# Kernel tuning notes

Measured on AMD Instinct MI355X. Metric: run time of the kernel, lower is better.

## Reference

```python
import jax, jax.numpy as jnp
import numpy as np

NEG_INF = -1e16


def setup_inputs() -> dict:
    key = jax.random.key(0)
    k1, k2, k3 = jax.random.split(key, 3)
    B, N, C, D = 8, 4096, 64, 64
    inputs = jax.random.normal(k1, (B, N, C), dtype=jnp.float32)
    graph = jax.random.randint(k2, (N, N), 0, 2, dtype=jnp.int32)
    # xavier_uniform for Linear weight [D, C]
    limit = float(np.sqrt(6.0 / (C + D)))
    W = jax.random.uniform(k3, (D, C), dtype=jnp.float32, minval=-limit, maxval=limit)
    b = jnp.zeros((D,), dtype=jnp.float32)
    return {"inputs": inputs, "graph": graph, "W": W, "b": b}


def reference(inputs, graph, W, b):
    # h = W(inputs): [B, N, D]
    h = jnp.einsum('bnc,dc->bnd', inputs, W)
    # dense pairwise scores: [B, N, N]
    scores = jnp.einsum('bnd,bmd->bnm', h, h)
    # mask non-edges (graph broadcasts over batch)
    scores = jnp.where(graph[None, :, :] == 0, NEG_INF, scores)
    attention = jax.nn.softmax(scores, axis=2)
    out = jnp.einsum('bnm,bmd->bnd', attention, h) + b
    return out
```

## Files before the change

kernel.cpp:

```cpp
#include <hip/hip_runtime.h>
#include <stdint.h>

typedef _Float16 f16x8 __attribute__((ext_vector_type(8)));
typedef _Float16 f16x4 __attribute__((ext_vector_type(4)));
typedef __fp16 half2_t __attribute__((ext_vector_type(2)));
typedef float f32x4 __attribute__((ext_vector_type(4)));

#define LOG2E 1.44269504088896340736f
#define NEGINF (-1e16f)

constexpr int kN = 4096;
constexpr int kD = 64;
constexpr int kB = 8;

__global__ __launch_bounds__(256) void hproj_kernel(const float* __restrict__ x,
                                                    const float* __restrict__ W,
                                                    _Float16* __restrict__ hout,
                                                    _Float16* __restrict__ hTout)
{
    __shared__ float Wt[64][64];
    __shared__ float xs[64][65];
    __shared__ _Float16 ht[64][68];

    const int tid = threadIdx.x;
    const int r   = tid >> 2;
    const int c0  = (tid & 3) * 16;

    #pragma unroll
    for (int j = 0; j < 16; j += 4) {
        const float4 v = *(const float4*)(W + r * 64 + c0 + j);
        Wt[c0 + j + 0][r] = v.x;
        Wt[c0 + j + 1][r] = v.y;
        Wt[c0 + j + 2][r] = v.z;
        Wt[c0 + j + 3][r] = v.w;
    }
    const long rowbase = (long)blockIdx.x * 64;
    #pragma unroll
    for (int j = 0; j < 16; j += 4) {
        const float4 v = *(const float4*)(x + (rowbase + r) * 64 + c0 + j);
        xs[r][c0 + j + 0] = v.x;
        xs[r][c0 + j + 1] = v.y;
        xs[r][c0 + j + 2] = v.z;
        xs[r][c0 + j + 3] = v.w;
    }
    __syncthreads();

    const int d0 = (tid & 3) * 16;
    f32x4 acc[4] = {{0.f,0.f,0.f,0.f},{0.f,0.f,0.f,0.f},{0.f,0.f,0.f,0.f},{0.f,0.f,0.f,0.f}};
    #pragma unroll 4
    for (int c = 0; c < 64; ++c) {
        const float xv = xs[r][c];
        const f32x4* wrow = (const f32x4*)&Wt[c][d0];
        #pragma unroll
        for (int k = 0; k < 4; ++k) acc[k] += wrow[k] * xv;
    }
    f16x8 o0, o1;
    #pragma unroll
    for (int j = 0; j < 8; ++j) {
        o0[j] = (_Float16)acc[j >> 2][j & 3];
        o1[j] = (_Float16)acc[2 + (j >> 2)][j & 3];
    }
    *(f16x8*)(hout + (rowbase + r) * 64 + d0)     = o0;
    *(f16x8*)(hout + (rowbase + r) * 64 + d0 + 8) = o1;

    #pragma unroll
    for (int j = 0; j < 8; ++j) {
        ht[r][d0 + j]     = o0[j];
        ht[r][d0 + 8 + j] = o1[j];
    }
    __syncthreads();

    const int bb = blockIdx.x >> 6;
    const int n0 = (int)(rowbase & (kN - 1));
    const int dr = tid >> 2;
    const int c4 = (tid & 3) * 16;
    f16x8 t0, t1;
    #pragma unroll
    for (int j = 0; j < 8; ++j) {
        t0[j] = ht[c4 + j][dr];
        t1[j] = ht[c4 + 8 + j][dr];
    }
    _Float16* dst = hTout + (long)bb * kD * kN + (long)dr * kN + n0 + c4;
    *(f16x8*)(dst)     = t0;
    *(f16x8*)(dst + 8) = t1;
}

__global__ __launch_bounds__(256) void graphmask_kernel(const int* __restrict__ g,
                                                        uint64_t* __restrict__ wmout)
{
    const int tid  = threadIdx.x;
    const int wv   = tid >> 6;
    const int lane = tid & 63;
    const int ll   = lane & 15;
    const int lg   = lane >> 4;
    const int pair = blockIdx.x * 4 + wv;
    const int q16  = pair >> 6;
    const int kv64 = pair & 63;

    const int* gr = g + (long)(q16 * 16 + ll) * kN + kv64 * 64 + 8 * lg;
    const int4 u0 = *(const int4*)(gr);
    const int4 u1 = *(const int4*)(gr + 4);
    const int4 u2 = *(const int4*)(gr + 32);
    const int4 u3 = *(const int4*)(gr + 36);

    int gv[16];
    gv[0] = u0.x;  gv[1] = u0.y;  gv[2] = u0.z;  gv[3] = u0.w;
    gv[4] = u1.x;  gv[5] = u1.y;  gv[6] = u1.z;  gv[7] = u1.w;
    gv[8] = u2.x;  gv[9] = u2.y;  gv[10] = u2.z;  gv[11] = u2.w;
    gv[12] = u3.x; gv[13] = u3.y; gv[14] = u3.z;  gv[15] = u3.w;

    uint64_t Wb[16];
    #pragma unroll
    for (int s = 0; s < 16; ++s) {
        const int t = s >> 2, rr = s & 3;
        const int j = (t >= 2 ? 8 : 0) + 4 * (t & 1) + rr;
        Wb[s] = __ballot(gv[j] != 0);
    }

    const int s = lane;
    uint64_t a0 = (s & 1) ? Wb[1]  : Wb[0];
    uint64_t a1 = (s & 1) ? Wb[3]  : Wb[2];
    uint64_t a2 = (s & 1) ? Wb[5]  : Wb[4];
    uint64_t a3 = (s & 1) ? Wb[7]  : Wb[6];
    uint64_t a4 = (s & 1) ? Wb[9]  : Wb[8];
    uint64_t a5 = (s & 1) ? Wb[11] : Wb[10];
    uint64_t a6 = (s & 1) ? Wb[13] : Wb[12];
    uint64_t a7 = (s & 1) ? Wb[15] : Wb[14];
    uint64_t b0 = (s & 2) ? a1 : a0;
    uint64_t b1 = (s & 2) ? a3 : a2;
    uint64_t b2 = (s & 2) ? a5 : a4;
    uint64_t b3 = (s & 2) ? a7 : a6;
    uint64_t c0 = (s & 4) ? b1 : b0;
    uint64_t c1 = (s & 4) ? b3 : b2;
    uint64_t v  = (s & 8) ? c1 : c0;
    if (lane < 16) wmout[(long)pair * 16 + lane] = v;
}

__global__ __launch_bounds__(512, 4) void attn_kernel(const _Float16* __restrict__ h,
                                                      const _Float16* __restrict__ hT,
                                                      const uint64_t* __restrict__ wmask,
                                                      const float* __restrict__ bias,
                                                      float* __restrict__ outp,
                                                      _Float16* __restrict__ pO,
                                                      float* __restrict__ pml,
                                                      int kvlen)
{
    __shared__ alignas(16) char Kl[2][8192];
    __shared__ alignas(16) char Vt[2][8192];

    const int b     = blockIdx.y;
    const int split = blockIdx.z;
    const int q0    = blockIdx.x * 256;
    const int tid   = threadIdx.x;
    const int wave  = tid >> 6;
    const int lane  = tid & 63;
    const int lg    = lane >> 4;
    const int ll    = lane & 15;

    const _Float16* hb  = h  + (long)b * kN * kD;
    const _Float16* hTb = hT + (long)b * kD * kN;
    const int kv_base = split * kvlen;
    const int NT      = kvlen / 64;

    const int qA = q0 + wave * 32 + ll;
    const int qB = qA + 16;
    const f16x8 qfA0 = *(const f16x8*)(hb + qA * 64 + lg * 8);
    const f16x8 qfA1 = *(const f16x8*)(hb + qA * 64 + 32 + lg * 8);
    const f16x8 qfB0 = *(const f16x8*)(hb + qB * 64 + lg * 8);
    const f16x8 qfB1 = *(const f16x8*)(hb + qB * 64 + 32 + lg * 8);

    f16x8 vone;
    {
        const _Float16 o = (ll == 0) ? (_Float16)1.0f : (_Float16)0.0f;
        #pragma unroll
        for (int j = 0; j < 8; ++j) vone[j] = o;
    }

    f32x4 OaccA[4] = {{0.f,0.f,0.f,0.f},{0.f,0.f,0.f,0.f},{0.f,0.f,0.f,0.f},{0.f,0.f,0.f,0.f}};
    f32x4 OaccB[4] = {{0.f,0.f,0.f,0.f},{0.f,0.f,0.f,0.f},{0.f,0.f,0.f,0.f},{0.f,0.f,0.f,0.f}};
    f32x4 Oacc4A = {0.f, 0.f, 0.f, 0.f};
    f32x4 Oacc4B = {0.f, 0.f, 0.f, 0.f};
    float m_runA = NEGINF, m_runB = NEGINF;
    float mmA = NEGINF * LOG2E, mmB = NEGINF * LOG2E;
    float negv = NEGINF;

    const int sr  = tid >> 3;
    const int sc8 = (tid & 7) * 8;
    const int srp = (sr & 0x23) | ((sr & 0x18) >> 1) | ((sr & 0x4) << 2);

    const int kw = srp * 128 + ((sc8 * 2) ^ ((srp & 7) << 4));
    const int vw = sr  * 128 + ((sc8 * 2) ^ ((sr  & 7) << 4));
    const int rb0 = ll * 128 + (((lg * 16))      ^ ((ll & 7) << 4));
    const int rb1 = ll * 128 + (((64 + lg * 16)) ^ ((ll & 7) << 4));

    char* const KB = (char*)Kl;
    char* const VB = (char*)Vt;

    const _Float16* gK = hb  + (long)(kv_base + sr) * 64 + sc8;
    const _Float16* gV = hTb + (long)sr * kN + kv_base + sc8;

    const int wuni = __builtin_amdgcn_readfirstlane(wave);
    const uint64_t* __restrict__ wmpA =
        wmask + ((long)(blockIdx.x * 16 + wuni * 2) * 64 + (kv_base >> 6)) * 16;
    const uint64_t* __restrict__ wmpB = wmpA + (long)64 * 16;

    {
        const f16x8 a0 = *(const f16x8*)(gK);
        const f16x8 b0 = *(const f16x8*)(gV);
        *(f16x8*)(KB + kw) = a0;
        *(f16x8*)(VB + vw) = b0;
        gK += 64 * 64;  gV += 64;
    }

    union PF { half2_t hh[4]; f16x8 v; };

#define SOFTMAX_FRAG(S_, WM_, OACC_, OACC4_, MRUN_, MM_, PF1_, PF2_)             \
    do {                                                                         \
        _Pragma("unroll")                                                        \
        for (int t = 0; t < 4; ++t) {                                            \
            _Pragma("unroll")                                                    \
            for (int rr = 0; rr < 4; ++rr) {                                     \
                float sv = S_[t][rr];                                            \
                asm("v_cndmask_b32 %0, %1, %2, %3"                               \
                    : "=v"(sv) : "v"(negv), "v"(sv), "s"(WM_[t * 4 + rr]));      \
                S_[t][rr] = sv;                                                  \
            }                                                                    \
        }                                                                        \
        float mx0 = fmaxf(fmaxf(S_[0][0], S_[0][1]), fmaxf(S_[0][2], S_[0][3])); \
        float mx1 = fmaxf(fmaxf(S_[1][0], S_[1][1]), fmaxf(S_[1][2], S_[1][3])); \
        float mx2 = fmaxf(fmaxf(S_[2][0], S_[2][1]), fmaxf(S_[2][2], S_[2][3])); \
        float mx3 = fmaxf(fmaxf(S_[3][0], S_[3][1]), fmaxf(S_[3][2], S_[3][3])); \
        float mloc = fmaxf(fmaxf(mx0, mx1), fmaxf(mx2, mx3));                    \
        mloc = fmaxf(mloc, __shfl_xor(mloc, 16));                                \
        mloc = fmaxf(mloc, __shfl_xor(mloc, 32));                                \
        if (__any(mloc > MRUN_ + 8.f)) {                                         \
            const float mnew = fmaxf(MRUN_, mloc);                               \
            const float scl  = __builtin_amdgcn_exp2f((MRUN_ - mnew) * LOG2E);   \
            MRUN_ = mnew;                                                        \
            MM_   = mnew * LOG2E;                                                \
            _Pragma("unroll")                                                    \
            for (int dt = 0; dt < 4; ++dt) OACC_[dt] *= scl;                     \
            OACC4_ *= scl;                                                       \
        }                                                                        \
        _Pragma("unroll")                                                        \
        for (int t = 0; t < 4; ++t) {                                            \
            _Pragma("unroll")                                                    \
            for (int rr = 0; rr < 4; ++rr)                                       \
                S_[t][rr] = __builtin_amdgcn_exp2f(fmaf(S_[t][rr], LOG2E, -MM_));\
        }                                                                        \
        PF1_.hh[0] = __builtin_amdgcn_cvt_pkrtz(S_[0][0], S_[0][1]);             \
        PF1_.hh[1] = __builtin_amdgcn_cvt_pkrtz(S_[0][2], S_[0][3]);             \
        PF1_.hh[2] = __builtin_amdgcn_cvt_pkrtz(S_[1][0], S_[1][1]);             \
        PF1_.hh[3] = __builtin_amdgcn_cvt_pkrtz(S_[1][2], S_[1][3]);             \
        PF2_.hh[0] = __builtin_amdgcn_cvt_pkrtz(S_[2][0], S_[2][1]);             \
        PF2_.hh[1] = __builtin_amdgcn_cvt_pkrtz(S_[2][2], S_[2][3]);             \
        PF2_.hh[2] = __builtin_amdgcn_cvt_pkrtz(S_[3][0], S_[3][1]);             \
        PF2_.hh[3] = __builtin_amdgcn_cvt_pkrtz(S_[3][2], S_[3][3]);             \
    } while (0)

#define TILE_BODY(IT, CB, NB)                                                    \
    do {                                                                         \
        const int it_ = (IT);                                                    \
                  \
        f16x8 nk0{}, nv0{};                                                      \
        if (it_ + 1 < NT) {                                                      \
            nk0 = *(const f16x8*)(gK);                                           \
            nv0 = *(const f16x8*)(gV);                                           \
            gK += 64 * 64;  gV += 64;                                            \
        }                                                                        \
                         \
        asm volatile("s_waitcnt lgkmcnt(0)" ::: "memory");                       \
        __builtin_amdgcn_s_barrier();                                            \
        __builtin_amdgcn_sched_barrier(0);                                       \
                \
        uint64_t WMA[16], WMB[16];                                               \
        _Pragma("unroll")                                                        \
        for (int s5 = 0; s5 < 16; ++s5) WMA[s5] = wmpA[(long)it_ * 16 + s5];     \
        _Pragma("unroll")                                                        \
        for (int s5 = 0; s5 < 16; ++s5) WMB[s5] = wmpB[(long)it_ * 16 + s5];     \
                                       \
        f32x4 SA[4], SB[4];                                                      \
        __builtin_amdgcn_s_setprio(1);                                           \
        _Pragma("unroll")                                                        \
        for (int t = 0; t < 4; ++t) {                                            \
            const f16x8 k0 = *(const f16x8*)(KB + (CB) + rb0 + t * 2048);        \
            const f16x8 k1 = *(const f16x8*)(KB + (CB) + rb1 + t * 2048);        \
            f32x4 sa = {0.f, 0.f, 0.f, 0.f};                                     \
            f32x4 sb = {0.f, 0.f, 0.f, 0.f};                                     \
            sa = __builtin_amdgcn_mfma_f32_16x16x32_f16(k0, qfA0, sa, 0, 0, 0);  \
            sa = __builtin_amdgcn_mfma_f32_16x16x32_f16(k1, qfA1, sa, 0, 0, 0);  \
            sb = __builtin_amdgcn_mfma_f32_16x16x32_f16(k0, qfB0, sb, 0, 0, 0);  \
            sb = __builtin_amdgcn_mfma_f32_16x16x32_f16(k1, qfB1, sb, 0, 0, 0);  \
            SA[t] = sa;                                                          \
            SB[t] = sb;                                                          \
        }                                                                        \
        __builtin_amdgcn_s_setprio(0);                                           \
                                  \
        if (it_ + 1 < NT) {                                                      \
            *(f16x8*)(KB + (NB) + kw) = nk0;                                     \
            *(f16x8*)(VB + (NB) + vw) = nv0;                                     \
        }                                                                        \
        PF pfA1, pfA2, pfB1, pfB2;                                               \
        SOFTMAX_FRAG(SA, WMA, OaccA, Oacc4A, m_runA, mmA, pfA1, pfA2);           \
        SOFTMAX_FRAG(SB, WMB, OaccB, Oacc4B, m_runB, mmB, pfB1, pfB2);           \
                                       \
        __builtin_amdgcn_s_setprio(1);                                           \
        _Pragma("unroll")                                                        \
        for (int dt = 0; dt < 4; ++dt) {                                         \
            const f16x8 v0 = *(const f16x8*)(VB + (CB) + rb0 + dt * 2048);       \
            const f16x8 v1 = *(const f16x8*)(VB + (CB) + rb1 + dt * 2048);       \
            OaccA[dt] = __builtin_amdgcn_mfma_f32_16x16x32_f16(v0, pfA1.v, OaccA[dt], 0, 0, 0); \
            OaccA[dt] = __builtin_amdgcn_mfma_f32_16x16x32_f16(v1, pfA2.v, OaccA[dt], 0, 0, 0); \
            OaccB[dt] = __builtin_amdgcn_mfma_f32_16x16x32_f16(v0, pfB1.v, OaccB[dt], 0, 0, 0); \
            OaccB[dt] = __builtin_amdgcn_mfma_f32_16x16x32_f16(v1, pfB2.v, OaccB[dt], 0, 0, 0); \
        }                                                                        \
        Oacc4A = __builtin_amdgcn_mfma_f32_16x16x32_f16(vone, pfA1.v, Oacc4A, 0, 0, 0); \
        Oacc4A = __builtin_amdgcn_mfma_f32_16x16x32_f16(vone, pfA2.v, Oacc4A, 0, 0, 0); \
        Oacc4B = __builtin_amdgcn_mfma_f32_16x16x32_f16(vone, pfB1.v, Oacc4B, 0, 0, 0); \
        Oacc4B = __builtin_amdgcn_mfma_f32_16x16x32_f16(vone, pfB2.v, Oacc4B, 0, 0, 0); \
        __builtin_amdgcn_s_setprio(0);                                           \
    } while (0)

    for (int ith = 0; ith < NT; ith += 2) {
        TILE_BODY(ith,     0,    8192);
        TILE_BODY(ith + 1, 8192, 0);
    }
#undef TILE_BODY
#undef SOFTMAX_FRAG

    const float lsumA = __shfl(Oacc4A[0], ll, 64);
    const float lsumB = __shfl(Oacc4B[0], ll, 64);
    const float invA  = (lsumA > 0.f) ? (1.0f / lsumA) : 0.f;
    const float invB  = (lsumB > 0.f) ? (1.0f / lsumB) : 0.f;

    if (outp != nullptr) {
        #pragma unroll
        for (int dt = 0; dt < 4; ++dt) {
            const int dbase = dt * 16 + lg * 4;
            const f32x4 bv = *(const f32x4*)(bias + dbase);
            f32x4 oa, ob;
            #pragma unroll
            for (int rr = 0; rr < 4; ++rr) {
                oa[rr] = OaccA[dt][rr] * invA + bv[rr];
                ob[rr] = OaccB[dt][rr] * invB + bv[rr];
            }
            *(f32x4*)(outp + ((long)b * kN + qA) * 64 + dbase) = oa;
            *(f32x4*)(outp + ((long)b * kN + qB) * 64 + dbase) = ob;
        }
    } else {
        const long srowA = (long)split * kB * kN + (long)b * kN + qA;
        const long srowB = srowA + 16;
        #pragma unroll
        for (int dt = 0; dt < 4; ++dt) {
            const int dbase = dt * 16 + lg * 4;
            f16x4 pa, pb;
            #pragma unroll
            for (int rr = 0; rr < 4; ++rr) {
                pa[rr] = (_Float16)(OaccA[dt][rr] * invA);
                pb[rr] = (_Float16)(OaccB[dt][rr] * invB);
            }
            *(f16x4*)(pO + srowA * 64 + dbase) = pa;
            *(f16x4*)(pO + srowB * 64 + dbase) = pb;
        }
        if (lane < 16) {
            pml[srowA * 2 + 0] = m_runA;
            pml[srowA * 2 + 1] = lsumA;
            pml[srowB * 2 + 0] = m_runB;
            pml[srowB * 2 + 1] = lsumB;
        }
    }
}

__global__ __launch_bounds__(256) void combine_kernel(const _Float16* __restrict__ pO,
                                                      const float* __restrict__ pml,
                                                      const float* __restrict__ bias,
                                                      float* __restrict__ outp,
                                                      int ks)
{
    const long idx = (long)blockIdx.x * 256 + threadIdx.x;
    const long row = idx >> 4;
    const int  d4  = (int)(idx & 15) * 4;

    float M = NEGINF;
    for (int s = 0; s < ks; ++s)
        M = fmaxf(M, pml[((long)s * kB * kN + row) * 2]);

    float L = 0.f;
    f32x4 acc = {0.f, 0.f, 0.f, 0.f};
    for (int s = 0; s < ks; ++s) {
        const long srow = (long)s * kB * kN + row;
        const float m = pml[srow * 2 + 0];
        const float l = pml[srow * 2 + 1];
        const float w = l * __builtin_amdgcn_exp2f((m - M) * LOG2E);
        L += w;
        const f16x4 o = *(const f16x4*)(pO + srow * 64 + d4);
        #pragma unroll
        for (int j = 0; j < 4; ++j) acc[j] += (float)o[j] * w;
    }
    const float invL = (L > 0.f) ? (1.0f / L) : 0.f;
    const f32x4 bv = *(const f32x4*)(bias + d4);
    *(f32x4*)(outp + row * 64 + d4) = acc * invL + bv;
}

extern "C" void kernel_launch(void* const* d_in, const int* in_sizes, int n_in,
                              void* d_out, int out_size, void* d_ws, size_t ws_size,
                              hipStream_t stream) {
    const float*  x     = (const float*)d_in[0];
    const int*    graph = (const int*)d_in[1];
    const float*  W     = (const float*)d_in[2];
    const float*  bias  = (const float*)d_in[3];
    float*        outp  = (float*)d_out;

    char* ws = (char*)d_ws;
    _Float16* hptr  = (_Float16*)ws;
    _Float16* hTptr = (_Float16*)(ws + (4u << 20));
    uint64_t* wmptr = (uint64_t*)(ws + (8u << 20));

    int ks = 1;
    if      (ws_size >= ((size_t)28 << 20)) ks = 4;
    else if (ws_size >= ((size_t)19 << 20)) ks = 2;

    _Float16* pO  = (_Float16*)(ws + (10u << 20));
    float*    pml = (float*)(ws + (10u << 20) + (size_t)ks * (4u << 20));

    hproj_kernel<<<dim3(kB * kN / 64), dim3(256), 0, stream>>>(x, W, hptr, hTptr);
    graphmask_kernel<<<dim3(256 * 64 / 4), dim3(256), 0, stream>>>(graph, wmptr);

    if (ks == 1) {
        attn_kernel<<<dim3(kN / 256, kB, 1), dim3(512), 0, stream>>>(
            hptr, hTptr, wmptr, bias, outp, nullptr, nullptr, kN);
    } else {
        attn_kernel<<<dim3(kN / 256, kB, ks), dim3(512), 0, stream>>>(
            hptr, hTptr, wmptr, bias, nullptr, pO, pml, kN / ks);
        combine_kernel<<<dim3(kB * kN * 16 / 256), dim3(256), 0, stream>>>(
            pO, pml, bias, outp, ks);
    }
}
```

Measured before the change: 80.96 us.

## Fuse graph masking into attention kernel, reading int graph directly

Removes the separate graph-to-bitmask kernel and has the attention kernel load the raw int32 adjacency rows per tile, applying the mask with a select. This drops one launch and the bitmask workspace, shrinking the workspace thresholds for the split-KV path. In exchange, each batch re-reads the 64 MB int graph instead of a compact bitmask, which greatly increases global memory traffic and register use in the inner loop.

After: 234.3 us. +189.4%, slower.

```diff
diff --git a/kernel.cpp b/kernel.cpp
--- a/kernel.cpp
+++ b/kernel.cpp
@@ -85,60 +85,9 @@
     *(f16x8*)(dst + 8) = t1;
 }
 
-__global__ __launch_bounds__(256) void graphmask_kernel(const int* __restrict__ g,
-                                                        uint64_t* __restrict__ wmout)
-{
-    const int tid  = threadIdx.x;
-    const int wv   = tid >> 6;
-    const int lane = tid & 63;
-    const int ll   = lane & 15;
-    const int lg   = lane >> 4;
-    const int pair = blockIdx.x * 4 + wv;
-    const int q16  = pair >> 6;
-    const int kv64 = pair & 63;
-
-    const int* gr = g + (long)(q16 * 16 + ll) * kN + kv64 * 64 + 8 * lg;
-    const int4 u0 = *(const int4*)(gr);
-    const int4 u1 = *(const int4*)(gr + 4);
-    const int4 u2 = *(const int4*)(gr + 32);
-    const int4 u3 = *(const int4*)(gr + 36);
-
-    int gv[16];
-    gv[0] = u0.x;  gv[1] = u0.y;  gv[2] = u0.z;  gv[3] = u0.w;
-    gv[4] = u1.x;  gv[5] = u1.y;  gv[6] = u1.z;  gv[7] = u1.w;
-    gv[8] = u2.x;  gv[9] = u2.y;  gv[10] = u2.z;  gv[11] = u2.w;
-    gv[12] = u3.x; gv[13] = u3.y; gv[14] = u3.z;  gv[15] = u3.w;
-
-    uint64_t Wb[16];
-    #pragma unroll
-    for (int s = 0; s < 16; ++s) {
-        const int t = s >> 2, rr = s & 3;
-        const int j = (t >= 2 ? 8 : 0) + 4 * (t & 1) + rr;
-        Wb[s] = __ballot(gv[j] != 0);
-    }
-
-    const int s = lane;
-    uint64_t a0 = (s & 1) ? Wb[1]  : Wb[0];
-    uint64_t a1 = (s & 1) ? Wb[3]  : Wb[2];
-    uint64_t a2 = (s & 1) ? Wb[5]  : Wb[4];
-    uint64_t a3 = (s & 1) ? Wb[7]  : Wb[6];
-    uint64_t a4 = (s & 1) ? Wb[9]  : Wb[8];
-    uint64_t a5 = (s & 1) ? Wb[11] : Wb[10];
-    uint64_t a6 = (s & 1) ? Wb[13] : Wb[12];
-    uint64_t a7 = (s & 1) ? Wb[15] : Wb[14];
-    uint64_t b0 = (s & 2) ? a1 : a0;
-    uint64_t b1 = (s & 2) ? a3 : a2;
-    uint64_t b2 = (s & 2) ? a5 : a4;
-    uint64_t b3 = (s & 2) ? a7 : a6;
-    uint64_t c0 = (s & 4) ? b1 : b0;
-    uint64_t c1 = (s & 4) ? b3 : b2;
-    uint64_t v  = (s & 8) ? c1 : c0;
-    if (lane < 16) wmout[(long)pair * 16 + lane] = v;
-}
-
 __global__ __launch_bounds__(512, 4) void attn_kernel(const _Float16* __restrict__ h,
                                                       const _Float16* __restrict__ hT,
-                                                      const uint64_t* __restrict__ wmask,
+                                                      const int* __restrict__ graph,
                                                       const float* __restrict__ bias,
                                                       float* __restrict__ outp,
                                                       _Float16* __restrict__ pO,
@@ -182,7 +131,6 @@
     f32x4 Oacc4B = {0.f, 0.f, 0.f, 0.f};
     float m_runA = NEGINF, m_runB = NEGINF;
     float mmA = NEGINF * LOG2E, mmB = NEGINF * LOG2E;
-    float negv = NEGINF;
 
     const int sr  = tid >> 3;
     const int sc8 = (tid & 7) * 8;
@@ -199,10 +147,8 @@
     const _Float16* gK = hb  + (long)(kv_base + sr) * 64 + sc8;
     const _Float16* gV = hTb + (long)sr * kN + kv_base + sc8;
 
-    const int wuni = __builtin_amdgcn_readfirstlane(wave);
-    const uint64_t* __restrict__ wmpA =
-        wmask + ((long)(blockIdx.x * 16 + wuni * 2) * 64 + (kv_base >> 6)) * 16;
-    const uint64_t* __restrict__ wmpB = wmpA + (long)64 * 16;
+    const int* gqA = graph + (long)qA * kN + kv_base + 8 * lg;
+    const int* gqB = graph + (long)qB * kN + kv_base + 8 * lg;
 
     {
         const f16x8 a0 = *(const f16x8*)(gK);
@@ -214,16 +160,14 @@
 
     union PF { half2_t hh[4]; f16x8 v; };
 
-#define SOFTMAX_FRAG(S_, WM_, OACC_, OACC4_, MRUN_, MM_, PF1_, PF2_)             \
+#define SOFTMAX_FRAG(S_, GM_, OACC_, OACC4_, MRUN_, MM_, PF1_, PF2_)             \
     do {                                                                         \
         _Pragma("unroll")                                                        \
         for (int t = 0; t < 4; ++t) {                                            \
             _Pragma("unroll")                                                    \
             for (int rr = 0; rr < 4; ++rr) {                                     \
-                float sv = S_[t][rr];                                            \
-                asm("v_cndmask_b32 %0, %1, %2, %3"                               \
-                    : "=v"(sv) : "v"(negv), "v"(sv), "s"(WM_[t * 4 + rr]));      \
-                S_[t][rr] = sv;                                                  \
+                const int j = (t >= 2 ? 8 : 0) + 4 * (t & 1) + rr;               \
+                S_[t][rr] = GM_[j] ? S_[t][rr] : NEGINF;                         \
             }                                                                    \
         }                                                                        \
         float mx0 = fmaxf(fmaxf(S_[0][0], S_[0][1]), fmaxf(S_[0][2], S_[0][3])); \
@@ -261,7 +205,17 @@
 #define TILE_BODY(IT, CB, NB)                                                    \
     do {                                                                         \
         const int it_ = (IT);                                                    \
-                  \
+             \
+        const int4 mA0 = *(const int4*)(gqA);                                    \
+        const int4 mA1 = *(const int4*)(gqA + 4);                                \
+        const int4 mA2 = *(const int4*)(gqA + 32);                               \
+        const int4 mA3 = *(const int4*)(gqA + 36);                               \
+        const int4 mB0 = *(const int4*)(gqB);                                    \
+        const int4 mB1 = *(const int4*)(gqB + 4);                                \
+        const int4 mB2 = *(const int4*)(gqB + 32);                               \
+        const int4 mB3 = *(const int4*)(gqB + 36);                               \
+        gqA += 64;  gqB += 64;                                                   \
+                             \
         f16x8 nk0{}, nv0{};                                                      \
         if (it_ + 1 < NT) {                                                      \
             nk0 = *(const f16x8*)(gK);                                           \
@@ -272,12 +226,6 @@
         asm volatile("s_waitcnt lgkmcnt(0)" ::: "memory");                       \
         __builtin_amdgcn_s_barrier();                                            \
         __builtin_amdgcn_sched_barrier(0);                                       \
-                \
-        uint64_t WMA[16], WMB[16];                                               \
-        _Pragma("unroll")                                                        \
-        for (int s5 = 0; s5 < 16; ++s5) WMA[s5] = wmpA[(long)it_ * 16 + s5];     \
-        _Pragma("unroll")                                                        \
-        for (int s5 = 0; s5 < 16; ++s5) WMB[s5] = wmpB[(long)it_ * 16 + s5];     \
                                        \
         f32x4 SA[4], SB[4];                                                      \
         __builtin_amdgcn_s_setprio(1);                                           \
@@ -300,9 +248,19 @@
             *(f16x8*)(KB + (NB) + kw) = nk0;                                     \
             *(f16x8*)(VB + (NB) + vw) = nv0;                                     \
         }                                                                        \
+                          \
+        int gmA[16], gmB[16];                                                    \
+        gmA[0]=mA0.x; gmA[1]=mA0.y; gmA[2]=mA0.z; gmA[3]=mA0.w;                  \
+        gmA[4]=mA1.x; gmA[5]=mA1.y; gmA[6]=mA1.z; gmA[7]=mA1.w;                  \
+        gmA[8]=mA2.x; gmA[9]=mA2.y; gmA[10]=mA2.z; gmA[11]=mA2.w;                \
+        gmA[12]=mA3.x; gmA[13]=mA3.y; gmA[14]=mA3.z; gmA[15]=mA3.w;              \
+        gmB[0]=mB0.x; gmB[1]=mB0.y; gmB[2]=mB0.z; gmB[3]=mB0.w;                  \
+        gmB[4]=mB1.x; gmB[5]=mB1.y; gmB[6]=mB1.z; gmB[7]=mB1.w;                  \
+        gmB[8]=mB2.x; gmB[9]=mB2.y; gmB[10]=mB2.z; gmB[11]=mB2.w;                \
+        gmB[12]=mB3.x; gmB[13]=mB3.y; gmB[14]=mB3.z; gmB[15]=mB3.w;              \
         PF pfA1, pfA2, pfB1, pfB2;                                               \
-        SOFTMAX_FRAG(SA, WMA, OaccA, Oacc4A, m_runA, mmA, pfA1, pfA2);           \
-        SOFTMAX_FRAG(SB, WMB, OaccB, Oacc4B, m_runB, mmB, pfB1, pfB2);           \
+        SOFTMAX_FRAG(SA, gmA, OaccA, Oacc4A, m_runA, mmA, pfA1, pfA2);           \
+        SOFTMAX_FRAG(SB, gmB, OaccB, Oacc4B, m_runB, mmB, pfB1, pfB2);           \
                                        \
         __builtin_amdgcn_s_setprio(1);                                           \
         _Pragma("unroll")                                                        \
@@ -414,24 +372,22 @@
     char* ws = (char*)d_ws;
     _Float16* hptr  = (_Float16*)ws;
     _Float16* hTptr = (_Float16*)(ws + (4u << 20));
-    uint64_t* wmptr = (uint64_t*)(ws + (8u << 20));
 
     int ks = 1;
-    if      (ws_size >= ((size_t)28 << 20)) ks = 4;
-    else if (ws_size >= ((size_t)19 << 20)) ks = 2;
-
-    _Float16* pO  = (_Float16*)(ws + (10u << 20));
-    float*    pml = (float*)(ws + (10u << 20) + (size_t)ks * (4u << 20));
+    if      (ws_size >= ((size_t)26 << 20)) ks = 4;
+    else if (ws_size >= ((size_t)17 << 20)) ks = 2;
+
+    _Float16* pO  = (_Float16*)(ws + (8u << 20));
+    float*    pml = (float*)(ws + (8u << 20) + (size_t)ks * (4u << 20));
 
     hproj_kernel<<<dim3(kB * kN / 64), dim3(256), 0, stream>>>(x, W, hptr, hTptr);
-    graphmask_kernel<<<dim3(256 * 64 / 4), dim3(256), 0, stream>>>(graph, wmptr);
 
     if (ks == 1) {
         attn_kernel<<<dim3(kN / 256, kB, 1), dim3(512), 0, stream>>>(
-            hptr, hTptr, wmptr, bias, outp, nullptr, nullptr, kN);
+            hptr, hTptr, graph, bias, outp, nullptr, nullptr, kN);
     } else {
         attn_kernel<<<dim3(kN / 256, kB, ks), dim3(512), 0, stream>>>(
-            hptr, hTptr, wmptr, bias, nullptr, pO, pml, kN / ks);
+            hptr, hTptr, graph, bias, nullptr, pO, pml, kN / ks);
         combine_kernel<<<dim3(kB * kN * 16 / 256), dim3(256), 0, stream>>>(
             pO, pml, bias, outp, ks);
     }
```
